# Optimization experiments

Measured on AMD Instinct MI355X. Metric: run time of the kernel, lower is better.

Reference implementation:

```python
import jax, jax.numpy as jnp
import numpy as np

N_EMBD = 384
BLOCK_SIZE = 256
HEAD_SIZE = 384
B, T = 512, 256


def setup_inputs() -> dict:
    key = jax.random.key(0)
    k1, k2, k3, k4 = jax.random.split(key, 4)
    scale = 1.0 / np.sqrt(N_EMBD)
    return {
        "x": jax.random.normal(k1, (B, T, N_EMBD), dtype=jnp.float32),
        "Wq": jax.random.normal(k2, (N_EMBD, HEAD_SIZE), dtype=jnp.float32) * scale,
        "Wk": jax.random.normal(k3, (N_EMBD, HEAD_SIZE), dtype=jnp.float32) * scale,
        "Wv": jax.random.normal(k4, (N_EMBD, HEAD_SIZE), dtype=jnp.float32) * scale,
    }


def reference(x, Wq, Wk, Wv):
    # x: [B, T, C]; projections (bias-free linears)
    q = jnp.einsum('btc,ch->bth', x, Wq)  # [B, T, H]
    k = jnp.einsum('btc,ch->bth', x, Wk)
    v = jnp.einsum('btc,ch->bth', x, Wv)
    scale = k.shape[-1] ** -0.5
    scores = jnp.einsum('bth,bsh->bts', q, k) * scale  # [B, T, T]
    t = q.shape[1]
    causal = jnp.tril(jnp.ones((t, t), dtype=bool))
    scores = jnp.where(causal, scores, -jnp.inf)
    attn = jax.nn.softmax(scores, axis=-1)
    # dropout omitted (eval mode / deterministic reference)
    out = jnp.einsum('bts,bsh->bth', attn, v)  # [B, T, H]
    return out
```

## Files before the change

kernel.cpp:

```cpp
#include <hip/hip_runtime.h>

#define Bn 512
#define Tn 256
#define Cn 384
#define Hn 384
#define Mn (Bn*Tn)
#define N3 1152

typedef _Float16 f16x8 __attribute__((ext_vector_type(8)));
typedef float    f32x4 __attribute__((ext_vector_type(4)));
typedef unsigned short u16;
typedef unsigned int   u32;

__device__ inline u16 f2h(float f){
  _Float16 h = (_Float16)f;
  return __builtin_bit_cast(u16, h);
}

__device__ inline void gl_lds16(const void* g, void* l){
  __builtin_amdgcn_global_load_lds(
      (const __attribute__((address_space(1))) u32*)g,
      (__attribute__((address_space(3))) u32*)l, 16, 0, 0);
}

__global__ __launch_bounds__(256) void k_convert_x(const float* __restrict__ x,
                                                   u16* __restrict__ xh){
  const size_t i8 = (size_t)blockIdx.x*256 + threadIdx.x;
  const float4* xp = (const float4*)x;
  float4 a = xp[i8*2], b = xp[i8*2+1];
  union { uint4 u; u16 s[8]; } o;
  o.s[0]=f2h(a.x); o.s[1]=f2h(a.y); o.s[2]=f2h(a.z); o.s[3]=f2h(a.w);
  o.s[4]=f2h(b.x); o.s[5]=f2h(b.y); o.s[6]=f2h(b.z); o.s[7]=f2h(b.w);
  ((uint4*)xh)[i8] = o.u;
}

__global__ __launch_bounds__(256) void k_convert_w(const float* __restrict__ Wq,
                                                   const float* __restrict__ Wk,
                                                   const float* __restrict__ Wv,
                                                   u16* __restrict__ wt3){
  const int idx = blockIdx.x*256 + threadIdx.x;
  const int n = idx / 384, c = idx % 384;
  const int w = n / 384, h = n % 384;
  const float* W = (w == 0) ? Wk : (w == 1) ? Wv : Wq;
  const float qscale = 1.4426950408889634f * rsqrtf(384.0f);
  const float sc = (w == 2) ? qscale : 1.0f;
  wt3[idx] = f2h(W[c*384 + h] * sc);
}

__global__ __launch_bounds__(256) void k_gemm(const u16* __restrict__ xh,
                                              const u16* __restrict__ wt3,
                                              u16* __restrict__ y){
  __shared__ u16 As[128*32];
  __shared__ u16 Bs[128*32];
  const int tid = threadIdx.x;
  const int lane = tid & 63, wv = tid >> 6;
  const int wu = (blockIdx.x & 7) * 1152 + (blockIdx.x >> 3);
  const int m0 = (wu / 9) * 128;
  const int n0 = (wu % 9) * 128;
  const int wrow = (wv & 1) * 64, wcol = (wv >> 1) * 64;
  const int q = lane >> 4, c = lane & 15;

  f32x4 acc[4][4];
#pragma unroll
  for (int i = 0; i < 4; ++i)
#pragma unroll
    for (int j = 0; j < 4; ++j) acc[i][j] = (f32x4){0.f,0.f,0.f,0.f};

  const char* xb = (const char*)xh;
  const char* wb = (const char*)wt3;

  for (int ks = 0; ks < 12; ++ks){
    const int k0 = ks * 32;
#pragma unroll
    for (int j = 0; j < 2; ++j){
      const int flat = j*4096 + wv*1024 + lane*16;
      const int row = flat >> 6, cb = flat & 63;
      gl_lds16(xb + (size_t)(m0+row)*768 + k0*2 + cb, (char*)As + j*4096 + wv*1024);
      gl_lds16(wb + (size_t)(n0+row)*768 + k0*2 + cb, (char*)Bs + j*4096 + wv*1024);
    }
    __syncthreads();
    f16x8 a[4], b[4];
#pragma unroll
    for (int i = 0; i < 4; ++i)
      a[i] = *(const f16x8*)&As[(wrow + i*16 + c)*32 + q*8];
#pragma unroll
    for (int j = 0; j < 4; ++j)
      b[j] = *(const f16x8*)&Bs[(wcol + j*16 + c)*32 + q*8];
#pragma unroll
    for (int i = 0; i < 4; ++i)
#pragma unroll
      for (int j = 0; j < 4; ++j)
        acc[i][j] = __builtin_amdgcn_mfma_f32_16x16x32_f16(a[i], b[j], acc[i][j], 0, 0, 0);
    __syncthreads();
  }
#pragma unroll
  for (int i = 0; i < 4; ++i)
#pragma unroll
    for (int j = 0; j < 4; ++j)
#pragma unroll
      for (int r = 0; r < 4; ++r){
        const int m = m0 + wrow + i*16 + q*4 + r;
        const int n = n0 + wcol + j*16 + c;
        y[(size_t)m*N3 + n] = f2h(acc[i][j][r]);
      }
}

__global__ __launch_bounds__(256) void k_transpose(const u16* __restrict__ y,
                                                   u16* __restrict__ vT){
  __shared__ u16 s[64*64];
  const int tid = threadIdx.x;
  const int blk = blockIdx.x;
  const int hb = blk % 6, tb = (blk/6) & 3, b = blk / 24;
  const int t0 = tb*64, h0 = hb*64;
#pragma unroll
  for (int it = 0; it < 2; ++it){
    const int flat = it*4096 + tid*16;
    const int tr = flat >> 7;
    const int he = (flat & 127) >> 1;
    union { uint4 u; u16 v[8]; } d;
    d.u = *(const uint4*)(y + (size_t)(b*Tn + t0 + tr)*N3 + 384 + h0 + he);
    const int hb3 = he >> 3;
#pragma unroll
    for (int e = 0; e < 8; ++e){
      const int h = he + e;
      s[h*64 + (tr & 7) + 8*((tr >> 3) ^ hb3)] = d.v[e];
    }
  }
  __syncthreads();
#pragma unroll
  for (int it = 0; it < 2; ++it){
    const int flat = it*4096 + tid*16;
    const int hr = flat >> 7;
    const int te = (flat & 127) >> 1;
    const int blkx = (te >> 3) ^ ((hr >> 3) & 7);
    uint4 d = *(const uint4*)&s[hr*64 + blkx*8];
    *(uint4*)(vT + (size_t)b*Hn*Tn + (size_t)(h0+hr)*Tn + t0 + te) = d;
  }
}

__global__ __launch_bounds__(512, 2) void k_attn(const u16* __restrict__ y,
                                                 const u16* __restrict__ vT,
                                                 float* __restrict__ out){
  __shared__ u16 Ks[64*384];
  __shared__ u16 Vs[384*64];
  __shared__ u16 ps_all[8][16*72];
  const int tid = threadIdx.x;
  const int lane = tid & 63, wv = tid >> 6;
  const int xcd = blockIdx.x & 7, lix = blockIdx.x >> 3;
  const int qt = (lix < 64) ? 1 : 0;
  const int b = xcd*64 + (lix & 63);
  const int t0 = qt*128 + wv*16;
  const u16* yb = y  + (size_t)b*Tn*N3;
  const u16* vb = vT + (size_t)b*Hn*Tn;
  u16* ps = ps_all[wv];
  const int q = lane >> 4, c = lane & 15;

  f16x8 qf[12];
#pragma unroll
  for (int kk = 0; kk < 12; ++kk)
    qf[kk] = *(const f16x8*)(yb + (size_t)(t0 + c)*N3 + 768 + kk*32 + q*8);

  f32x4 accO[24];
#pragma unroll
  for (int n = 0; n < 24; ++n) accO[n] = (f32x4){0.f,0.f,0.f,0.f};
  float m_i[4] = {-1e30f,-1e30f,-1e30f,-1e30f};
  float l_i[4] = {0.f,0.f,0.f,0.f};

  const int nst = qt*2 + 2;

  auto stageK = [&](int s0){
#pragma unroll
    for (int it = 0; it < 6; ++it){
      const int slot = it*512 + tid;
      const int r = slot / 48, gs = slot % 48;
      const int g = (gs & ~7) | ((gs & 7) ^ (r & 7));
      gl_lds16(yb + (size_t)(s0 + r)*N3 + g*8, (char*)Ks + (it*8 + wv)*1024);
    }
  };
  auto stageV = [&](int s0){
#pragma unroll
    for (int it = 0; it < 6; ++it){
      const int slot = it*512 + tid;
      const int h = slot >> 3, gsv = slot & 7;
      const int g = gsv ^ (h & 7);
      gl_lds16(vb + (size_t)h*Tn + s0 + g*8, (char*)Vs + (it*8 + wv)*1024);
    }
  };

  stageK(0);
  stageV(0);
  asm volatile("s_waitcnt vmcnt(6)" ::: "memory");
  __builtin_amdgcn_s_barrier();
  asm volatile("" ::: "memory");

  for (int st = 0; st < nst; ++st){
    const int s0 = st*64;
    const bool active = (s0 <= t0 + 15);

    if (active){
      f32x4 accS[4];
#pragma unroll
      for (int j = 0; j < 4; ++j) accS[j] = (f32x4){0.f,0.f,0.f,0.f};
#pragma unroll
      for (int kk = 0; kk < 12; ++kk){
#pragma unroll
        for (int j = 0; j < 4; ++j){
          const int s = j*16 + c;
          const int g = kk*4 + q;
          const int gs = (g & ~7) | ((g & 7) ^ (c & 7));
          const f16x8 bf = *(const f16x8*)&Ks[(s*48 + gs)*8];
          accS[j] = __builtin_amdgcn_mfma_f32_16x16x32_f16(qf[kk], bf, accS[j], 0, 0, 0);
        }
      }

      if (s0 + 63 > t0){
#pragma unroll
        for (int j = 0; j < 4; ++j){
          const int s = s0 + j*16 + c;
#pragma unroll
          for (int i = 0; i < 4; ++i)
            if (s > t0 + q*4 + i) accS[j][i] = -1e30f;
        }
      }
      float alpha[4];
#pragma unroll
      for (int i = 0; i < 4; ++i){
        float mx = fmaxf(fmaxf(accS[0][i], accS[1][i]), fmaxf(accS[2][i], accS[3][i]));
#pragma unroll
        for (int d = 1; d < 16; d <<= 1) mx = fmaxf(mx, __shfl_xor(mx, d, 64));
        const float mnew = fmaxf(m_i[i], mx);
        alpha[i] = exp2f(m_i[i] - mnew);
        m_i[i] = mnew;
        float sum = 0.f;
#pragma unroll
        for (int j = 0; j < 4; ++j){
          const float p = exp2f(accS[j][i] - mnew);
          accS[j][i] = p;
          sum += p;
        }
#pragma unroll
        for (int d = 1; d < 16; d <<= 1) sum += __shfl_xor(sum, d, 64);
        l_i[i] = l_i[i]*alpha[i] + sum;
      }
#pragma unroll
      for (int j = 0; j < 4; ++j)
#pragma unroll
        for (int i = 0; i < 4; ++i)
          ps[(q*4 + i)*72 + j*16 + c] = f2h(accS[j][i]);
#pragma unroll
      for (int n = 0; n < 24; ++n)
#pragma unroll
        for (int i = 0; i < 4; ++i) accO[n][i] *= alpha[i];
    }

    __builtin_amdgcn_s_barrier();
    asm volatile("" ::: "memory");
    if (st + 1 < nst){
      stageK(s0 + 64);
      asm volatile("s_waitcnt vmcnt(6)" ::: "memory");
    } else {
      asm volatile("s_waitcnt vmcnt(0)" ::: "memory");
    }
    __builtin_amdgcn_s_barrier();
    asm volatile("" ::: "memory");

    if (active){
#pragma unroll
      for (int kk = 0; kk < 2; ++kk){
        const f16x8 af = *(const f16x8*)&ps[c*72 + kk*32 + q*8];
#pragma unroll
        for (int n = 0; n < 24; ++n){
          const int h = n*16 + c;
          const int gs = (kk*4 + q) ^ (c & 7);
          const f16x8 bf = *(const f16x8*)&Vs[(h*8 + gs)*8];
          accO[n] = __builtin_amdgcn_mfma_f32_16x16x32_f16(af, bf, accO[n], 0, 0, 0);
        }
      }
    }

    __builtin_amdgcn_s_barrier();
    asm volatile("" ::: "memory");
    if (st + 1 < nst){
      stageV(s0 + 64);
      asm volatile("s_waitcnt vmcnt(6)" ::: "memory");
      __builtin_amdgcn_s_barrier();
      asm volatile("" ::: "memory");
    }
  }

#pragma unroll
  for (int i = 0; i < 4; ++i){
    const float r = 1.f / l_i[i];
    float* op = out + ((size_t)b*Tn + t0 + q*4 + i)*Hn;
#pragma unroll
    for (int n = 0; n < 24; ++n)
      op[n*16 + c] = accO[n][i] * r;
  }
}

extern "C" void kernel_launch(void* const* d_in, const int* in_sizes, int n_in,
                              void* d_out, int out_size, void* d_ws, size_t ws_size,
                              hipStream_t stream){
  (void)in_sizes; (void)n_in; (void)out_size; (void)ws_size;
  const float* x  = (const float*)d_in[0];
  const float* Wq = (const float*)d_in[1];
  const float* Wk = (const float*)d_in[2];
  const float* Wv = (const float*)d_in[3];
  float* out = (float*)d_out;
  char* ws = (char*)d_ws;

  u16* xh  = (u16*)ws;
  u16* yq  = (u16*)(ws + (size_t)Mn*Cn*2);
  u16* wt3 = (u16*)(ws + (size_t)Mn*Cn*2 + (size_t)Mn*N3*2);
  u16* vT  = xh;

  k_convert_x<<<24576, 256, 0, stream>>>(x, xh);
  k_convert_w<<<1728,  256, 0, stream>>>(Wq, Wk, Wv, wt3);
  k_gemm     <<<9216,  256, 0, stream>>>(xh, wt3, yq);
  k_transpose<<<12288, 256, 0, stream>>>(yq, vT);
  k_attn     <<<1024,  512, 0, stream>>>(yq, vT, out);
}
```

Before: 724.0 us.

## Triple-buffer QKV GEMM loads with swizzled LDS and raise MFMA priority

```diff
diff --git a/kernel.cpp b/kernel.cpp
--- a/kernel.cpp
+++ b/kernel.cpp
@@ -47,11 +47,11 @@
   wt3[idx] = f2h(W[c*384 + h] * sc);
 }
 
-__global__ __launch_bounds__(256) void k_gemm(const u16* __restrict__ xh,
-                                              const u16* __restrict__ wt3,
-                                              u16* __restrict__ y){
-  __shared__ u16 As[128*32];
-  __shared__ u16 Bs[128*32];
+__global__ __launch_bounds__(256, 3) void k_gemm(const u16* __restrict__ xh,
+                                                 const u16* __restrict__ wt3,
+                                                 u16* __restrict__ y){
+  __shared__ u16 As[3][128*32];
+  __shared__ u16 Bs[3][128*32];
   const int tid = threadIdx.x;
   const int lane = tid & 63, wv = tid >> 6;
   const int wu = (blockIdx.x & 7) * 1152 + (blockIdx.x >> 3);
@@ -69,29 +69,52 @@
   const char* xb = (const char*)xh;
   const char* wb = (const char*)wt3;
 
-  for (int ks = 0; ks < 12; ++ks){
-    const int k0 = ks * 32;
+  auto stage = [&](int buf, int ks){
 #pragma unroll
     for (int j = 0; j < 2; ++j){
       const int flat = j*4096 + wv*1024 + lane*16;
-      const int row = flat >> 6, cb = flat & 63;
-      gl_lds16(xb + (size_t)(m0+row)*768 + k0*2 + cb, (char*)As + j*4096 + wv*1024);
-      gl_lds16(wb + (size_t)(n0+row)*768 + k0*2 + cb, (char*)Bs + j*4096 + wv*1024);
-    }
-    __syncthreads();
+      const int row = flat >> 6;
+      const int gb = (flat >> 4) & 3;
+      const int g = gb ^ ((row & 3) ^ ((row >> 2) & 3));
+      gl_lds16(xb + (size_t)(m0+row)*768 + ks*64 + g*16, (char*)As[buf] + flat);
+      gl_lds16(wb + (size_t)(n0+row)*768 + ks*64 + g*16, (char*)Bs[buf] + flat);
+    }
+  };
+
+  stage(0, 0);
+  stage(1, 1);
+  stage(2, 2);
+  asm volatile("s_waitcnt vmcnt(8)" ::: "memory");
+  __builtin_amdgcn_s_barrier();
+  asm volatile("" ::: "memory");
+
+  const int vsw = (c & 3) ^ ((c >> 2) & 3);
+#pragma unroll
+  for (int t = 0; t < 12; ++t){
+    const int cur = t % 3;
     f16x8 a[4], b[4];
 #pragma unroll
     for (int i = 0; i < 4; ++i)
-      a[i] = *(const f16x8*)&As[(wrow + i*16 + c)*32 + q*8];
+      a[i] = *(const f16x8*)&As[cur][(wrow + i*16 + c)*32 + ((q ^ vsw)*8)];
 #pragma unroll
     for (int j = 0; j < 4; ++j)
-      b[j] = *(const f16x8*)&Bs[(wcol + j*16 + c)*32 + q*8];
+      b[j] = *(const f16x8*)&Bs[cur][(wcol + j*16 + c)*32 + ((q ^ vsw)*8)];
+    __builtin_amdgcn_s_setprio(1);
 #pragma unroll
     for (int i = 0; i < 4; ++i)
 #pragma unroll
       for (int j = 0; j < 4; ++j)
         acc[i][j] = __builtin_amdgcn_mfma_f32_16x16x32_f16(a[i], b[j], acc[i][j], 0, 0, 0);
-    __syncthreads();
+    __builtin_amdgcn_s_setprio(0);
+    if (t == 11) break;
+    __builtin_amdgcn_s_barrier();
+    asm volatile("" ::: "memory");
+    if (t + 3 < 12) stage(cur, t + 3);
+    if (t < 9)       asm volatile("s_waitcnt vmcnt(8)" ::: "memory");
+    else if (t == 9) asm volatile("s_waitcnt vmcnt(4)" ::: "memory");
+    else             asm volatile("s_waitcnt vmcnt(0)" ::: "memory");
+    __builtin_amdgcn_s_barrier();
+    asm volatile("" ::: "memory");
   }
 #pragma unroll
   for (int i = 0; i < 4; ++i)
@@ -201,6 +224,7 @@
       f32x4 accS[4];
 #pragma unroll
       for (int j = 0; j < 4; ++j) accS[j] = (f32x4){0.f,0.f,0.f,0.f};
+      __builtin_amdgcn_s_setprio(1);
 #pragma unroll
       for (int kk = 0; kk < 12; ++kk){
 #pragma unroll
@@ -212,6 +236,7 @@
           accS[j] = __builtin_amdgcn_mfma_f32_16x16x32_f16(qf[kk], bf, accS[j], 0, 0, 0);
         }
       }
+      __builtin_amdgcn_s_setprio(0);
 
       if (s0 + 63 > t0){
 #pragma unroll
@@ -265,6 +290,7 @@
     asm volatile("" ::: "memory");
 
     if (active){
+      __builtin_amdgcn_s_setprio(1);
 #pragma unroll
       for (int kk = 0; kk < 2; ++kk){
         const f16x8 af = *(const f16x8*)&ps[c*72 + kk*32 + q*8];
@@ -276,6 +302,7 @@
           accO[n] = __builtin_amdgcn_mfma_f32_16x16x32_f16(af, bf, accO[n], 0, 0, 0);
         }
       }
+      __builtin_amdgcn_s_setprio(0);
     }
 
     __builtin_amdgcn_s_barrier();
```

Result: no change. 718.9 us (-0.7%).
